# Performance work log

Hardware: AMD Instinct MI355X
Metric: run time of the kernel (lower is better)

## Reference

```python
import jax, jax.numpy as jnp
import numpy as np

B, N, F = 512, 2048, 64
T = 4            # number of atom types
H1, H2 = 64, 32  # hidden widths; final layer outputs 1 (per-atom energy)


def setup_inputs() -> dict:
    key = jax.random.key(0)
    ks = jax.random.split(key, 8)
    x = jax.random.normal(ks[0], (B, N, F), dtype=jnp.float32)
    atomic_numbers = jax.random.randint(ks[1], (N,), 0, T)
    s = 0.05
    # Per-type MLP parameters, stacked over the type axis (torch Linear layout: [out, in]).
    w0 = jax.random.normal(ks[2], (T, H1, F), dtype=jnp.float32) * s
    b0 = jax.random.normal(ks[3], (T, H1), dtype=jnp.float32) * s
    w1 = jax.random.normal(ks[4], (T, H2, H1), dtype=jnp.float32) * s
    b1 = jax.random.normal(ks[5], (T, H2), dtype=jnp.float32) * s
    w2 = jax.random.normal(ks[6], (T, 1, H2), dtype=jnp.float32) * s
    b2 = jax.random.normal(ks[7], (T, 1), dtype=jnp.float32) * s
    return {"x": x, "atomic_numbers": atomic_numbers,
            "w0": w0, "b0": b0, "w1": w1, "b1": b1, "w2": w2, "b2": b2}


def reference(x, atomic_numbers, w0, b0, w1, b1, w2, b2):
    # Behler-Parrinello: route each atom through the MLP of its atom type,
    # then sum per-atom energies over atoms.  The torch version gathers atoms
    # by type, runs each type's MLP, and scatters back; here we evaluate all
    # T type-MLPs batched over the type axis and select with a one-hot mask
    # (identical math, jit-friendly, no data-dependent shapes).
    onehot = jax.nn.one_hot(atomic_numbers, w0.shape[0], dtype=x.dtype)  # [N, T]
    h = jax.nn.silu(jnp.einsum('bnf,thf->tbnh', x, w0) + b0[:, None, None, :])   # [T,B,N,H1]
    h = jax.nn.silu(jnp.einsum('tbnh,tgh->tbng', h, w1) + b1[:, None, None, :])  # [T,B,N,H2]
    e = jnp.einsum('tbng,tog->tbno', h, w2) + b2[:, None, None, :]               # [T,B,N,1]
    e = e[..., 0]                                                                # [T,B,N]
    per_atom = jnp.einsum('tbn,nt->bn', e, onehot)  # select the matching type per atom
    return per_atom.sum(axis=-1)                    # [B]
```

## Files before the change

### kernel.cpp

```cpp
#include <hip/hip_runtime.h>
#include <hip/hip_bf16.h>


#define B_ 512
#define N_ 2048
#define F_ 64
#define T_ 4
#define H1_ 64
#define H2_ 32

#define BT 16
#define WAVES 4
#define NCHUNK 64
#define SLICE (NCHUNK / WAVES)

typedef __attribute__((ext_vector_type(8))) short bf16x8;
typedef __attribute__((ext_vector_type(4))) short bf16x4;
typedef __attribute__((ext_vector_type(4))) float f32x4;

__device__ inline float silu_f(float v) {
    return v * __builtin_amdgcn_rcpf(1.0f + __expf(-v));
}

__device__ inline bf16x8 pack8(float4 a, float4 b) {
    union { __hip_bfloat162 h[4]; bf16x8 v; } u;
    u.h[0] = __float22bfloat162_rn({a.x, a.y});
    u.h[1] = __float22bfloat162_rn({a.z, a.w});
    u.h[2] = __float22bfloat162_rn({b.x, b.y});
    u.h[3] = __float22bfloat162_rn({b.z, b.w});
    return u.v;
}

__device__ inline bf16x4 pack4(float a, float b, float c, float d) {
    union { __hip_bfloat162 h[2]; bf16x4 v; } u;
    u.h[0] = __float22bfloat162_rn({a, b});
    u.h[1] = __float22bfloat162_rn({c, d});
    return u.v;
}

__device__ inline float bf_at(bf16x4 v, int r) {
    union { bf16x4 v; __hip_bfloat16 h[4]; } u; u.v = v;
    return __bfloat162float(u.h[r]);
}

__global__ __launch_bounds__(256, 3) void bpnn_kernel(
    const float* __restrict__ x, const int* __restrict__ an,
    const float* __restrict__ w0, const float* __restrict__ b0,
    const float* __restrict__ w1, const float* __restrict__ b1,
    const float* __restrict__ w2, const float* __restrict__ b2,
    float* __restrict__ out)
{
    __shared__ __align__(16) __hip_bfloat16 trb[WAVES][BT][68];
    __shared__ int sidx[NCHUNK];
    __shared__ int cnt[T_], pos[T_];
    __shared__ float red[BT];

    const int tid  = threadIdx.x;
    const int wave = tid >> 6;
    const int lane = tid & 63;
    const int lr   = lane & 15;
    const int q    = lane >> 4;
    const int b0i  = blockIdx.y * BT;
    const int n0   = blockIdx.x * NCHUNK;

    if (tid < T_)  cnt[tid] = 0;
    if (tid < BT)  red[tid] = 0.0f;
    __syncthreads();
    int myt = 0;
    if (tid < NCHUNK) { myt = an[n0 + tid]; atomicAdd(&cnt[myt], 1); }
    __syncthreads();
    if (tid == 0) {
        int o = 0;
        for (int k = 0; k < T_; ++k) { pos[k] = o; o += cnt[k]; }
    }
    __syncthreads();
    if (tid < NCHUNK) { int p = atomicAdd(&pos[myt], 1); sidx[p] = (myt << 8) | tid; }
    __syncthreads();

    bf16x8 aw0[4][2], aw1[2][2];
    bf16x4 b0f[4], b1f[2], w2f[2];
    float b2cur = 0.0f;
    int cur_t = -1;

    auto load_frags = [&](int t) {
        const float* w0t = w0 + t * (H1_ * F_);
        const float* w1t = w1 + t * (H2_ * H1_);
#pragma unroll
        for (int nt = 0; nt < 4; ++nt)
#pragma unroll
            for (int kh = 0; kh < 2; ++kh) {
                const float4* p = reinterpret_cast<const float4*>(
                    w0t + (nt * 16 + lr) * F_ + kh * 32 + q * 8);
                aw0[nt][kh] = pack8(p[0], p[1]);
            }
#pragma unroll
        for (int mt = 0; mt < 2; ++mt)
#pragma unroll
            for (int kh = 0; kh < 2; ++kh) {
                const float4* p = reinterpret_cast<const float4*>(
                    w1t + (mt * 16 + lr) * H1_ + kh * 32 + q * 8);
                aw1[mt][kh] = pack8(p[0], p[1]);
            }
#pragma unroll
        for (int nt = 0; nt < 4; ++nt) {
            float4 v = *reinterpret_cast<const float4*>(b0 + t * H1_ + nt * 16 + q * 4);
            b0f[nt] = pack4(v.x, v.y, v.z, v.w);
        }
#pragma unroll
        for (int mt = 0; mt < 2; ++mt) {
            float4 v = *reinterpret_cast<const float4*>(b1 + t * H2_ + mt * 16 + q * 4);
            b1f[mt] = pack4(v.x, v.y, v.z, v.w);
            float4 u = *reinterpret_cast<const float4*>(w2 + t * H2_ + mt * 16 + q * 4);
            w2f[mt] = pack4(u.x, u.y, u.z, u.w);
        }
        b2cur = b2[t];
    };

    const float* xb_ = x + (size_t)(b0i + lr) * (N_ * F_) + (size_t)n0 * F_ + q * 8;
    __hip_bfloat16* trbw = &trb[wave][lr][0];

    float esum0 = 0.f, esum1 = 0.f, bsum = 0.f;

    auto compute = [&](bf16x8 xf0, bf16x8 xf1) {
        f32x4 acc[4] = {{0,0,0,0},{0,0,0,0},{0,0,0,0},{0,0,0,0}};
#pragma unroll
        for (int nt = 0; nt < 4; ++nt) {
            acc[nt] = __builtin_amdgcn_mfma_f32_16x16x32_bf16(aw0[nt][0], xf0, acc[nt], 0, 0, 0);
            acc[nt] = __builtin_amdgcn_mfma_f32_16x16x32_bf16(aw0[nt][1], xf1, acc[nt], 0, 0, 0);
        }
#pragma unroll
        for (int nt = 0; nt < 4; ++nt) {
            float v0 = silu_f(acc[nt][0] + bf_at(b0f[nt], 0));
            float v1 = silu_f(acc[nt][1] + bf_at(b0f[nt], 1));
            float v2 = silu_f(acc[nt][2] + bf_at(b0f[nt], 2));
            float v3 = silu_f(acc[nt][3] + bf_at(b0f[nt], 3));
            *reinterpret_cast<bf16x4*>(trbw + nt * 16 + q * 4) = pack4(v0, v1, v2, v3);
        }
        __builtin_amdgcn_wave_barrier();

        bf16x8 hb0 = *reinterpret_cast<const bf16x8*>(trbw + q * 8);
        bf16x8 hb1 = *reinterpret_cast<const bf16x8*>(trbw + 32 + q * 8);
        __builtin_amdgcn_wave_barrier();

        f32x4 accB[2] = {{0,0,0,0},{0,0,0,0}};
#pragma unroll
        for (int mt = 0; mt < 2; ++mt) {
            accB[mt] = __builtin_amdgcn_mfma_f32_16x16x32_bf16(aw1[mt][0], hb0, accB[mt], 0, 0, 0);
            accB[mt] = __builtin_amdgcn_mfma_f32_16x16x32_bf16(aw1[mt][1], hb1, accB[mt], 0, 0, 0);
        }
#pragma unroll
        for (int r = 0; r < 4; ++r) {
            float v0 = silu_f(accB[0][r] + bf_at(b1f[0], r));
            esum0 += v0 * bf_at(w2f[0], r);
            float v1 = silu_f(accB[1][r] + bf_at(b1f[1], r));
            esum1 += v1 * bf_at(w2f[1], r);
        }
    };

    const int s0 = wave * SLICE, s1 = s0 + SLICE;

    int id0 = sidx[s0];
    int id1 = sidx[s0 + 1];
    float4 rA0, rA1, rA2, rA3, rB0, rB1, rB2, rB3;
    {
        const float4* pA = reinterpret_cast<const float4*>(xb_ + (id0 & 0xFF) * F_);
        rA0 = pA[0]; rA1 = pA[1]; rA2 = pA[8]; rA3 = pA[9];
        const float4* pB = reinterpret_cast<const float4*>(xb_ + (id1 & 0xFF) * F_);
        rB0 = pB[0]; rB1 = pB[1]; rB2 = pB[8]; rB3 = pB[9];
    }

    for (int p = s0; p < s1; p += 2) {
        int pc = (p + 2 < s1) ? p + 2 : s1 - 1;
        int pd = (p + 3 < s1) ? p + 3 : s1 - 1;
        int idn0 = sidx[pc];
        int idn1 = sidx[pd];

        int tA = id0 >> 8;
        if (tA != cur_t) { cur_t = tA; load_frags(tA); }
        bf16x8 xf0 = pack8(rA0, rA1);
        bf16x8 xf1 = pack8(rA2, rA3);
        {
            const float4* pn = reinterpret_cast<const float4*>(xb_ + (idn0 & 0xFF) * F_);
            rA0 = pn[0]; rA1 = pn[1]; rA2 = pn[8]; rA3 = pn[9];
        }
        bsum += b2cur;
        compute(xf0, xf1);

        int tB = id1 >> 8;
        if (tB != cur_t) { cur_t = tB; load_frags(tB); }
        bf16x8 yf0 = pack8(rB0, rB1);
        bf16x8 yf1 = pack8(rB2, rB3);
        {
            const float4* pn = reinterpret_cast<const float4*>(xb_ + (idn1 & 0xFF) * F_);
            rB0 = pn[0]; rB1 = pn[1]; rB2 = pn[8]; rB3 = pn[9];
        }
        bsum += b2cur;
        compute(yf0, yf1);

        id0 = idn0; id1 = idn1;
    }

    float esum = esum0 + esum1;
    esum += __shfl_xor(esum, 16);
    esum += __shfl_xor(esum, 32);
    if (q == 0) atomicAdd(&red[lr], esum + bsum);
    __syncthreads();
    if (tid < BT) atomicAdd(&out[b0i + tid], red[tid]);
}

extern "C" void kernel_launch(void* const* d_in, const int* in_sizes, int n_in,
                              void* d_out, int out_size, void* d_ws, size_t ws_size,
                              hipStream_t stream) {
    const float* x  = (const float*)d_in[0];
    const int*   an = (const int*)d_in[1];
    const float* w0 = (const float*)d_in[2];
    const float* b0 = (const float*)d_in[3];
    const float* w1 = (const float*)d_in[4];
    const float* b1 = (const float*)d_in[5];
    const float* w2 = (const float*)d_in[6];
    const float* b2 = (const float*)d_in[7];
    float* out = (float*)d_out;

    hipMemsetAsync(out, 0, B_ * sizeof(float), stream);
    dim3 grid(N_ / NCHUNK, B_ / BT);
    bpnn_kernel<<<grid, 256, 0, stream>>>(x, an, w0, b0, w1, b1, w2, b2, out);
}
```

Baseline: 448.6 us.

## Globally sort atoms by type in a pre-kernel so waves see uniform types

Adds a single-wave kernel that counting-sorts all atoms by type into a workspace array. The main kernel now takes contiguous slices of this global order, so each wave sees at most a few type changes and reloads its weight fragments only on a change. It drops the per-block shared-memory sort and its barriers. In exchange it adds a serial launch, and it gathers x rows from scattered atom indices across the whole N range, which may hurt memory locality.

```diff
diff --git a/kernel.cpp b/kernel.cpp
--- a/kernel.cpp
+++ b/kernel.cpp
@@ -43,16 +43,47 @@
     return __bfloat162float(u.h[r]);
 }
 
+__global__ void sort_atoms(const int* __restrict__ an, int* __restrict__ sorted) {
+    const int lane = threadIdx.x;
+    int v[32];
+#pragma unroll
+    for (int c = 0; c < 32; ++c) v[c] = an[c * 64 + lane];
+
+    int c0 = 0, c1 = 0, c2 = 0;
+#pragma unroll
+    for (int c = 0; c < 32; ++c) {
+        c0 += __popcll(__ballot(v[c] == 0));
+        c1 += __popcll(__ballot(v[c] == 1));
+        c2 += __popcll(__ballot(v[c] == 2));
+    }
+    int base0 = 0, base1 = c0, base2 = c0 + c1, base3 = c0 + c1 + c2;
+    const unsigned long long mb = (1ull << lane) - 1ull;
+#pragma unroll
+    for (int c = 0; c < 32; ++c) {
+        const int t = v[c];
+        unsigned long long m0 = __ballot(t == 0);
+        unsigned long long m1 = __ballot(t == 1);
+        unsigned long long m2 = __ballot(t == 2);
+        unsigned long long m3 = __ballot(t == 3);
+        int pos;
+        if (t == 0)      pos = base0 + (int)__popcll(m0 & mb);
+        else if (t == 1) pos = base1 + (int)__popcll(m1 & mb);
+        else if (t == 2) pos = base2 + (int)__popcll(m2 & mb);
+        else             pos = base3 + (int)__popcll(m3 & mb);
+        sorted[pos] = (t << 16) | (c * 64 + lane);
+        base0 += (int)__popcll(m0); base1 += (int)__popcll(m1);
+        base2 += (int)__popcll(m2); base3 += (int)__popcll(m3);
+    }
+}
+
 __global__ __launch_bounds__(256, 3) void bpnn_kernel(
-    const float* __restrict__ x, const int* __restrict__ an,
+    const float* __restrict__ x, const int* __restrict__ sorted,
     const float* __restrict__ w0, const float* __restrict__ b0,
     const float* __restrict__ w1, const float* __restrict__ b1,
     const float* __restrict__ w2, const float* __restrict__ b2,
     float* __restrict__ out)
 {
     __shared__ __align__(16) __hip_bfloat16 trb[WAVES][BT][68];
-    __shared__ int sidx[NCHUNK];
-    __shared__ int cnt[T_], pos[T_];
     __shared__ float red[BT];
 
     const int tid  = threadIdx.x;
@@ -61,143 +92,132 @@
     const int lr   = lane & 15;
     const int q    = lane >> 4;
     const int b0i  = blockIdx.y * BT;
-    const int n0   = blockIdx.x * NCHUNK;
-
-    if (tid < T_)  cnt[tid] = 0;
-    if (tid < BT)  red[tid] = 0.0f;
+
+    if (tid < BT) red[tid] = 0.0f;
     __syncthreads();
-    int myt = 0;
-    if (tid < NCHUNK) { myt = an[n0 + tid]; atomicAdd(&cnt[myt], 1); }
-    __syncthreads();
-    if (tid == 0) {
-        int o = 0;
-        for (int k = 0; k < T_; ++k) { pos[k] = o; o += cnt[k]; }
-    }
-    __syncthreads();
-    if (tid < NCHUNK) { int p = atomicAdd(&pos[myt], 1); sidx[p] = (myt << 8) | tid; }
-    __syncthreads();
-
-    bf16x8 aw0[4][2], aw1[2][2];
-    bf16x4 b0f[4], b1f[2], w2f[2];
-    float b2cur = 0.0f;
-    int cur_t = -1;
-
-    auto load_frags = [&](int t) {
-        const float* w0t = w0 + t * (H1_ * F_);
-        const float* w1t = w1 + t * (H2_ * H1_);
-#pragma unroll
-        for (int nt = 0; nt < 4; ++nt)
-#pragma unroll
-            for (int kh = 0; kh < 2; ++kh) {
-                const float4* p = reinterpret_cast<const float4*>(
-                    w0t + (nt * 16 + lr) * F_ + kh * 32 + q * 8);
-                aw0[nt][kh] = pack8(p[0], p[1]);
+
+    const float* xb_ = x + (size_t)(b0i + lr) * (N_ * F_) + q * 8;
+    __hip_bfloat16* trbw = &trb[wave][lr][0];
+
+    const int s0 = blockIdx.x * NCHUNK + wave * SLICE;
+    const int s1 = s0 + SLICE;
+
+    float esum0 = 0.f, esum1 = 0.f, bsum = 0.f;
+
+    bf16x8 aw000, aw001, aw010, aw011, aw020, aw021, aw030, aw031;
+    bf16x8 aw100, aw101, aw110, aw111;
+    bf16x4 b0f0, b0f1, b0f2, b0f3, b1f0, b1f1, w2f0, w2f1;
+    float b2c = 0.f;
+
+    int p = s0;
+    int id0 = __builtin_amdgcn_readfirstlane(sorted[p]);
+    int id1 = __builtin_amdgcn_readfirstlane(sorted[p + 1]);
+    float4 sa0, sa1, sa2, sa3, sb0, sb1, sb2, sb3;
+    {
+        const float4* pA = reinterpret_cast<const float4*>(xb_ + (id0 & 0xFFFF) * F_);
+        sa0 = pA[0]; sa1 = pA[1]; sa2 = pA[8]; sa3 = pA[9];
+        const float4* pB = reinterpret_cast<const float4*>(xb_ + (id1 & 0xFFFF) * F_);
+        sb0 = pB[0]; sb1 = pB[1]; sb2 = pB[8]; sb3 = pB[9];
+    }
+
+    while (p < s1) {
+        const int t = id0 >> 16;
+        {
+            const float* wb = w0 + t * (H1_ * F_) + lr * F_ + q * 8;
+            const float4* pw;
+            pw = reinterpret_cast<const float4*>(wb +  0 * F_ +  0); aw000 = pack8(pw[0], pw[1]);
+            pw = reinterpret_cast<const float4*>(wb +  0 * F_ + 32); aw001 = pack8(pw[0], pw[1]);
+            pw = reinterpret_cast<const float4*>(wb + 16 * F_ +  0); aw010 = pack8(pw[0], pw[1]);
+            pw = reinterpret_cast<const float4*>(wb + 16 * F_ + 32); aw011 = pack8(pw[0], pw[1]);
+            pw = reinterpret_cast<const float4*>(wb + 32 * F_ +  0); aw020 = pack8(pw[0], pw[1]);
+            pw = reinterpret_cast<const float4*>(wb + 32 * F_ + 32); aw021 = pack8(pw[0], pw[1]);
+            pw = reinterpret_cast<const float4*>(wb + 48 * F_ +  0); aw030 = pack8(pw[0], pw[1]);
+            pw = reinterpret_cast<const float4*>(wb + 48 * F_ + 32); aw031 = pack8(pw[0], pw[1]);
+            const float* wc = w1 + t * (H2_ * H1_) + lr * H1_ + q * 8;
+            pw = reinterpret_cast<const float4*>(wc +  0 * H1_ +  0); aw100 = pack8(pw[0], pw[1]);
+            pw = reinterpret_cast<const float4*>(wc +  0 * H1_ + 32); aw101 = pack8(pw[0], pw[1]);
+            pw = reinterpret_cast<const float4*>(wc + 16 * H1_ +  0); aw110 = pack8(pw[0], pw[1]);
+            pw = reinterpret_cast<const float4*>(wc + 16 * H1_ + 32); aw111 = pack8(pw[0], pw[1]);
+            float4 v;
+            v = *reinterpret_cast<const float4*>(b0 + t * H1_ +  0 + q * 4); b0f0 = pack4(v.x, v.y, v.z, v.w);
+            v = *reinterpret_cast<const float4*>(b0 + t * H1_ + 16 + q * 4); b0f1 = pack4(v.x, v.y, v.z, v.w);
+            v = *reinterpret_cast<const float4*>(b0 + t * H1_ + 32 + q * 4); b0f2 = pack4(v.x, v.y, v.z, v.w);
+            v = *reinterpret_cast<const float4*>(b0 + t * H1_ + 48 + q * 4); b0f3 = pack4(v.x, v.y, v.z, v.w);
+            v = *reinterpret_cast<const float4*>(b1 + t * H2_ +  0 + q * 4); b1f0 = pack4(v.x, v.y, v.z, v.w);
+            v = *reinterpret_cast<const float4*>(b1 + t * H2_ + 16 + q * 4); b1f1 = pack4(v.x, v.y, v.z, v.w);
+            v = *reinterpret_cast<const float4*>(w2 + t * H2_ +  0 + q * 4); w2f0 = pack4(v.x, v.y, v.z, v.w);
+            v = *reinterpret_cast<const float4*>(w2 + t * H2_ + 16 + q * 4); w2f1 = pack4(v.x, v.y, v.z, v.w);
+            b2c = b2[t];
+        }
+
+        for (;;) {
+            bf16x8 xf0 = pack8(sa0, sa1);
+            bf16x8 xf1 = pack8(sa2, sa3);
+            sa0 = sb0; sa1 = sb1; sa2 = sb2; sa3 = sb3;
+            int pn = p + 2;
+            int idn = id1;
+            if (pn < s1) idn = __builtin_amdgcn_readfirstlane(sorted[pn]);
+            {
+                const float4* pB = reinterpret_cast<const float4*>(xb_ + (idn & 0xFFFF) * F_);
+                sb0 = pB[0]; sb1 = pB[1]; sb2 = pB[8]; sb3 = pB[9];
             }
-#pragma unroll
-        for (int mt = 0; mt < 2; ++mt)
-#pragma unroll
-            for (int kh = 0; kh < 2; ++kh) {
-                const float4* p = reinterpret_cast<const float4*>(
-                    w1t + (mt * 16 + lr) * H1_ + kh * 32 + q * 8);
-                aw1[mt][kh] = pack8(p[0], p[1]);
+            bsum += b2c;
+
+            f32x4 acc0 = {0.f,0.f,0.f,0.f}, acc1 = {0.f,0.f,0.f,0.f};
+            f32x4 acc2 = {0.f,0.f,0.f,0.f}, acc3 = {0.f,0.f,0.f,0.f};
+            acc0 = __builtin_amdgcn_mfma_f32_16x16x32_bf16(aw000, xf0, acc0, 0, 0, 0);
+            acc0 = __builtin_amdgcn_mfma_f32_16x16x32_bf16(aw001, xf1, acc0, 0, 0, 0);
+            acc1 = __builtin_amdgcn_mfma_f32_16x16x32_bf16(aw010, xf0, acc1, 0, 0, 0);
+            acc1 = __builtin_amdgcn_mfma_f32_16x16x32_bf16(aw011, xf1, acc1, 0, 0, 0);
+            acc2 = __builtin_amdgcn_mfma_f32_16x16x32_bf16(aw020, xf0, acc2, 0, 0, 0);
+            acc2 = __builtin_amdgcn_mfma_f32_16x16x32_bf16(aw021, xf1, acc2, 0, 0, 0);
+            acc3 = __builtin_amdgcn_mfma_f32_16x16x32_bf16(aw030, xf0, acc3, 0, 0, 0);
+            acc3 = __builtin_amdgcn_mfma_f32_16x16x32_bf16(aw031, xf1, acc3, 0, 0, 0);
+
+            {
+                float v0 = silu_f(acc0[0] + bf_at(b0f0, 0));
+                float v1 = silu_f(acc0[1] + bf_at(b0f0, 1));
+                float v2 = silu_f(acc0[2] + bf_at(b0f0, 2));
+                float v3 = silu_f(acc0[3] + bf_at(b0f0, 3));
+                *reinterpret_cast<bf16x4*>(trbw +  0 + q * 4) = pack4(v0, v1, v2, v3);
+                v0 = silu_f(acc1[0] + bf_at(b0f1, 0));
+                v1 = silu_f(acc1[1] + bf_at(b0f1, 1));
+                v2 = silu_f(acc1[2] + bf_at(b0f1, 2));
+                v3 = silu_f(acc1[3] + bf_at(b0f1, 3));
+                *reinterpret_cast<bf16x4*>(trbw + 16 + q * 4) = pack4(v0, v1, v2, v3);
+                v0 = silu_f(acc2[0] + bf_at(b0f2, 0));
+                v1 = silu_f(acc2[1] + bf_at(b0f2, 1));
+                v2 = silu_f(acc2[2] + bf_at(b0f2, 2));
+                v3 = silu_f(acc2[3] + bf_at(b0f2, 3));
+                *reinterpret_cast<bf16x4*>(trbw + 32 + q * 4) = pack4(v0, v1, v2, v3);
+                v0 = silu_f(acc3[0] + bf_at(b0f3, 0));
+                v1 = silu_f(acc3[1] + bf_at(b0f3, 1));
+                v2 = silu_f(acc3[2] + bf_at(b0f3, 2));
+                v3 = silu_f(acc3[3] + bf_at(b0f3, 3));
+                *reinterpret_cast<bf16x4*>(trbw + 48 + q * 4) = pack4(v0, v1, v2, v3);
             }
-#pragma unroll
-        for (int nt = 0; nt < 4; ++nt) {
-            float4 v = *reinterpret_cast<const float4*>(b0 + t * H1_ + nt * 16 + q * 4);
-            b0f[nt] = pack4(v.x, v.y, v.z, v.w);
+            __builtin_amdgcn_wave_barrier();
+
+            bf16x8 hb0 = *reinterpret_cast<const bf16x8*>(trbw + q * 8);
+            bf16x8 hb1 = *reinterpret_cast<const bf16x8*>(trbw + 32 + q * 8);
+            __builtin_amdgcn_wave_barrier();
+
+            f32x4 acB0 = {0.f,0.f,0.f,0.f}, acB1 = {0.f,0.f,0.f,0.f};
+            acB0 = __builtin_amdgcn_mfma_f32_16x16x32_bf16(aw100, hb0, acB0, 0, 0, 0);
+            acB0 = __builtin_amdgcn_mfma_f32_16x16x32_bf16(aw101, hb1, acB0, 0, 0, 0);
+            acB1 = __builtin_amdgcn_mfma_f32_16x16x32_bf16(aw110, hb0, acB1, 0, 0, 0);
+            acB1 = __builtin_amdgcn_mfma_f32_16x16x32_bf16(aw111, hb1, acB1, 0, 0, 0);
+
+#pragma unroll
+            for (int r = 0; r < 4; ++r) {
+                esum0 += silu_f(acB0[r] + bf_at(b1f0, r)) * bf_at(w2f0, r);
+                esum1 += silu_f(acB1[r] + bf_at(b1f1, r)) * bf_at(w2f1, r);
+            }
+
+            ++p;
+            id0 = id1; id1 = idn;
+            if (p >= s1 || (id0 >> 16) != t) break;
         }
-#pragma unroll
-        for (int mt = 0; mt < 2; ++mt) {
-            float4 v = *reinterpret_cast<const float4*>(b1 + t * H2_ + mt * 16 + q * 4);
-            b1f[mt] = pack4(v.x, v.y, v.z, v.w);
-            float4 u = *reinterpret_cast<const float4*>(w2 + t * H2_ + mt * 16 + q * 4);
-            w2f[mt] = pack4(u.x, u.y, u.z, u.w);
-        }
-        b2cur = b2[t];
-    };
-
-    const float* xb_ = x + (size_t)(b0i + lr) * (N_ * F_) + (size_t)n0 * F_ + q * 8;
-    __hip_bfloat16* trbw = &trb[wave][lr][0];
-
-    float esum0 = 0.f, esum1 = 0.f, bsum = 0.f;
-
-    auto compute = [&](bf16x8 xf0, bf16x8 xf1) {
-        f32x4 acc[4] = {{0,0,0,0},{0,0,0,0},{0,0,0,0},{0,0,0,0}};
-#pragma unroll
-        for (int nt = 0; nt < 4; ++nt) {
-            acc[nt] = __builtin_amdgcn_mfma_f32_16x16x32_bf16(aw0[nt][0], xf0, acc[nt], 0, 0, 0);
-            acc[nt] = __builtin_amdgcn_mfma_f32_16x16x32_bf16(aw0[nt][1], xf1, acc[nt], 0, 0, 0);
-        }
-#pragma unroll
-        for (int nt = 0; nt < 4; ++nt) {
-            float v0 = silu_f(acc[nt][0] + bf_at(b0f[nt], 0));
-            float v1 = silu_f(acc[nt][1] + bf_at(b0f[nt], 1));
-            float v2 = silu_f(acc[nt][2] + bf_at(b0f[nt], 2));
-            float v3 = silu_f(acc[nt][3] + bf_at(b0f[nt], 3));
-            *reinterpret_cast<bf16x4*>(trbw + nt * 16 + q * 4) = pack4(v0, v1, v2, v3);
-        }
-        __builtin_amdgcn_wave_barrier();
-
-        bf16x8 hb0 = *reinterpret_cast<const bf16x8*>(trbw + q * 8);
-        bf16x8 hb1 = *reinterpret_cast<const bf16x8*>(trbw + 32 + q * 8);
-        __builtin_amdgcn_wave_barrier();
-
-        f32x4 accB[2] = {{0,0,0,0},{0,0,0,0}};
-#pragma unroll
-        for (int mt = 0; mt < 2; ++mt) {
-            accB[mt] = __builtin_amdgcn_mfma_f32_16x16x32_bf16(aw1[mt][0], hb0, accB[mt], 0, 0, 0);
-            accB[mt] = __builtin_amdgcn_mfma_f32_16x16x32_bf16(aw1[mt][1], hb1, accB[mt], 0, 0, 0);
-        }
-#pragma unroll
-        for (int r = 0; r < 4; ++r) {
-            float v0 = silu_f(accB[0][r] + bf_at(b1f[0], r));
-            esum0 += v0 * bf_at(w2f[0], r);
-            float v1 = silu_f(accB[1][r] + bf_at(b1f[1], r));
-            esum1 += v1 * bf_at(w2f[1], r);
-        }
-    };
-
-    const int s0 = wave * SLICE, s1 = s0 + SLICE;
-
-    int id0 = sidx[s0];
-    int id1 = sidx[s0 + 1];
-    float4 rA0, rA1, rA2, rA3, rB0, rB1, rB2, rB3;
-    {
-        const float4* pA = reinterpret_cast<const float4*>(xb_ + (id0 & 0xFF) * F_);
-        rA0 = pA[0]; rA1 = pA[1]; rA2 = pA[8]; rA3 = pA[9];
-        const float4* pB = reinterpret_cast<const float4*>(xb_ + (id1 & 0xFF) * F_);
-        rB0 = pB[0]; rB1 = pB[1]; rB2 = pB[8]; rB3 = pB[9];
-    }
-
-    for (int p = s0; p < s1; p += 2) {
-        int pc = (p + 2 < s1) ? p + 2 : s1 - 1;
-        int pd = (p + 3 < s1) ? p + 3 : s1 - 1;
-        int idn0 = sidx[pc];
-        int idn1 = sidx[pd];
-
-        int tA = id0 >> 8;
-        if (tA != cur_t) { cur_t = tA; load_frags(tA); }
-        bf16x8 xf0 = pack8(rA0, rA1);
-        bf16x8 xf1 = pack8(rA2, rA3);
-        {
-            const float4* pn = reinterpret_cast<const float4*>(xb_ + (idn0 & 0xFF) * F_);
-            rA0 = pn[0]; rA1 = pn[1]; rA2 = pn[8]; rA3 = pn[9];
-        }
-        bsum += b2cur;
-        compute(xf0, xf1);
-
-        int tB = id1 >> 8;
-        if (tB != cur_t) { cur_t = tB; load_frags(tB); }
-        bf16x8 yf0 = pack8(rB0, rB1);
-        bf16x8 yf1 = pack8(rB2, rB3);
-        {
-            const float4* pn = reinterpret_cast<const float4*>(xb_ + (idn1 & 0xFF) * F_);
-            rB0 = pn[0]; rB1 = pn[1]; rB2 = pn[8]; rB3 = pn[9];
-        }
-        bsum += b2cur;
-        compute(yf0, yf1);
-
-        id0 = idn0; id1 = idn1;
     }
 
     float esum = esum0 + esum1;
@@ -220,8 +240,10 @@
     const float* w2 = (const float*)d_in[6];
     const float* b2 = (const float*)d_in[7];
     float* out = (float*)d_out;
+    int* sorted = (int*)d_ws;
 
     hipMemsetAsync(out, 0, B_ * sizeof(float), stream);
+    sort_atoms<<<1, 64, 0, stream>>>(an, sorted);
     dim3 grid(N_ / NCHUNK, B_ / BT);
-    bpnn_kernel<<<grid, 256, 0, stream>>>(x, an, w0, b0, w1, b1, w2, b2, out);
-}
+    bpnn_kernel<<<grid, 256, 0, stream>>>(x, sorted, w0, b0, w1, b1, w2, b2, out);
+}
```

After: 397.5 us. -11.4%, faster.
